# Optimization experiments

Hardware: AMD Instinct MI355X
Metric: run time of the kernel (lower is better)

Reference implementation:

```python
import jax, jax.numpy as jnp
import numpy as np


def conv1x1(x, w, b):
    # x: [B,C,H,W], w: [O,C], b: [O] -> [B,O,H,W]
    return jnp.einsum('bchw,oc->bohw', x, w) + b[None, :, None, None]


def maxpool2x2(x):
    B, C, H, W = x.shape
    return x.reshape(B, C, H // 2, 2, W // 2, 2).max(axis=(3, 5))


def setup_inputs() -> dict:
    key = jax.random.key(0)
    ks = jax.random.split(key, 10)
    C = 256
    x = jax.random.normal(ks[0], (16, C, 64, 64), dtype=jnp.float32)
    s = lambda fan_in: 1.0 / np.sqrt(fan_in)
    w_theta = jax.random.normal(ks[1], (C // 8, C), dtype=jnp.float32) * s(C)
    b_theta = jax.random.normal(ks[2], (C // 8,), dtype=jnp.float32) * 0.01
    w_phi = jax.random.normal(ks[3], (C // 8, C), dtype=jnp.float32) * s(C)
    b_phi = jax.random.normal(ks[4], (C // 8,), dtype=jnp.float32) * 0.01
    w_g = jax.random.normal(ks[5], (C // 2, C), dtype=jnp.float32) * s(C)
    b_g = jax.random.normal(ks[6], (C // 2,), dtype=jnp.float32) * 0.01
    w_attn = jax.random.normal(ks[7], (C, C // 2), dtype=jnp.float32) * s(C // 2)
    b_attn = jax.random.normal(ks[8], (C,), dtype=jnp.float32) * 0.01
    sigma = jnp.full((1,), 0.5, dtype=jnp.float32)
    return {"x": x, "w_theta": w_theta, "b_theta": b_theta,
            "w_phi": w_phi, "b_phi": b_phi, "w_g": w_g, "b_g": b_g,
            "w_attn": w_attn, "b_attn": b_attn, "sigma": sigma}


def reference(x, w_theta, b_theta, w_phi, b_phi, w_g, b_g, w_attn, b_attn, sigma):
    B, C, W, H = x.shape
    N = W * H
    N4 = N // 4
    # Q: [B, N, C/8]
    theta = conv1x1(x, w_theta, b_theta).reshape(B, C // 8, N).transpose(0, 2, 1)
    # K: [B, C/8, N/4] (2x2 maxpool downsample)
    phi = maxpool2x2(conv1x1(x, w_phi, b_phi)).reshape(B, C // 8, N4)
    # attention: [B, N, N/4]
    attn = jax.nn.softmax(jnp.einsum('bnc,bcm->bnm', theta, phi), axis=-1)
    # V: [B, N/4, C/2]
    g = maxpool2x2(conv1x1(x, w_g, b_g)).reshape(B, C // 2, N4).transpose(0, 2, 1)
    attn_g = jnp.einsum('bnm,bmc->bnc', attn, g).transpose(0, 2, 1).reshape(B, C // 2, W, H)
    attn_g = conv1x1(attn_g, w_attn, b_attn)
    return x + sigma[0] * attn_g
```

## Files before the change

kernel.cpp:

```cpp
#include <hip/hip_runtime.h>
#include <math.h>

#define BATCH 16
#define CIN   256
#define NPIX  4096
#define NP4   1024
#define DQK   32
#define DV    128
#define KT    64
#define QW    32
#define QT    128

typedef __attribute__((ext_vector_type(8)))  short short8v;
typedef __attribute__((ext_vector_type(16))) float f32x16;

#define ZERO16 {0.f,0.f,0.f,0.f,0.f,0.f,0.f,0.f,0.f,0.f,0.f,0.f,0.f,0.f,0.f,0.f}
#define LOG2E 1.44269504088896340736f
#define MFIX 64.0f

__device__ __forceinline__ unsigned short f2bf(float f) {
    unsigned u = __float_as_uint(f);
    u += 0x7FFFu + ((u >> 16) & 1u);
    return (unsigned short)(u >> 16);
}

__device__ __forceinline__ unsigned cvtpk(float a, float b) {
    unsigned r;
    asm("v_cvt_pk_bf16_f32 %0, %1, %2" : "=v"(r) : "v"(a), "v"(b));
    return r;
}

__device__ __forceinline__ short8v ldg8(const unsigned short* p) {
    return *(const short8v*)p;
}

#define PLSWAP(a, b) asm("v_permlane32_swap_b32 %0, %1" : "+v"(a), "+v"(b))

__global__ void wcvt_k(const float* __restrict__ wt, const float* __restrict__ wp,
                       const float* __restrict__ wg, const float* __restrict__ wa,
                       unsigned short* __restrict__ wqkv, unsigned short* __restrict__ wab)
{
    int i = blockIdx.x * 256 + threadIdx.x;
    if (i < 192 * 256) {
        int row = i >> 8, c = i & 255;
        float v = row < 32 ? wt[row * 256 + c]
                : row < 64 ? wp[(row - 32) * 256 + c]
                           : wg[(row - 64) * 256 + c];
        wqkv[i] = f2bf(v);
    } else {
        int j = i - 192 * 256;
        if (j < 256 * DV) wab[j] = f2bf(wa[j]);
    }
}

__global__ __launch_bounds__(256, 2) void conv_qkv_k(
    const float* __restrict__ x, const unsigned short* __restrict__ wqkv,
    const float* __restrict__ b_theta, const float* __restrict__ b_phi,
    const float* __restrict__ b_g, unsigned short* __restrict__ Qg,
    unsigned short* __restrict__ Kg, unsigned short* __restrict__ Vg)
{
    __shared__ __align__(16) union {
        unsigned short xs[2][2][128][8];
        float pool[2][160][32];
    } u;

    const int b    = blockIdx.y;
    const int tile = blockIdx.x;
    const int pixb = tile * 128;
    const int t    = threadIdx.x;
    const int wv   = t >> 6, l = t & 63, h = l >> 5, q31 = l & 31;
    const int sp   = t & 127, skb = t >> 7;

    const float* xb = x + (size_t)b * CIN * NPIX + pixb + sp;

    f32x16 acc[6];
#pragma unroll
    for (int i = 0; i < 6; ++i) acc[i] = ZERO16;

    float xa[8], xbr[8];
#pragma unroll
    for (int j = 0; j < 8; ++j) xa[j] = xb[(size_t)(skb * 8 + j) * NPIX];
    {
        unsigned pk[4];
#pragma unroll
        for (int jj = 0; jj < 4; ++jj) pk[jj] = cvtpk(xa[2*jj], xa[2*jj+1]);
        *(uint4*)&u.xs[0][skb][sp][0] = *(uint4*)pk;
    }
#pragma unroll
    for (int j = 0; j < 8; ++j) xbr[j] = xb[(size_t)(16 + skb * 8 + j) * NPIX];
    __syncthreads();

    for (int ks = 0; ks < 16; ks += 2) {
        if (ks < 14) {
            const float* xn = xb + (size_t)((ks + 2) * 16 + skb * 8) * NPIX;
#pragma unroll
            for (int j = 0; j < 8; ++j) xa[j] = xn[(size_t)j * NPIX];
        }
        {
            short8v bf = *(const short8v*)&u.xs[0][h][wv * 32 + q31][0];
#pragma unroll
            for (int rb = 0; rb < 6; ++rb) {
                short8v af = *(const short8v*)&wqkv[(size_t)(rb * 32 + q31) * 256 + ks * 16 + h * 8];
                acc[rb] = __builtin_amdgcn_mfma_f32_32x32x16_bf16(af, bf, acc[rb], 0, 0, 0);
            }
        }
        {
            unsigned pk[4];
#pragma unroll
            for (int jj = 0; jj < 4; ++jj) pk[jj] = cvtpk(xbr[2*jj], xbr[2*jj+1]);
            *(uint4*)&u.xs[1][skb][sp][0] = *(uint4*)pk;
        }
        __syncthreads();

        if (ks < 14) {
            const float* xn = xb + (size_t)((ks + 3) * 16 + skb * 8) * NPIX;
#pragma unroll
            for (int j = 0; j < 8; ++j) xbr[j] = xn[(size_t)j * NPIX];
        }
        {
            short8v bf = *(const short8v*)&u.xs[1][h][wv * 32 + q31][0];
#pragma unroll
            for (int rb = 0; rb < 6; ++rb) {
                short8v af = *(const short8v*)&wqkv[(size_t)(rb * 32 + q31) * 256 + (ks + 1) * 16 + h * 8];
                acc[rb] = __builtin_amdgcn_mfma_f32_32x32x16_bf16(af, bf, acc[rb], 0, 0, 0);
            }
        }
        if (ks < 14) {
            unsigned pk[4];
#pragma unroll
            for (int jj = 0; jj < 4; ++jj) pk[jj] = cvtpk(xa[2*jj], xa[2*jj+1]);
            *(uint4*)&u.xs[0][skb][sp][0] = *(uint4*)pk;
        }
        __syncthreads();
    }

    {
        int pix = pixb + wv * 32 + q31;
        unsigned short* qout = &Qg[((size_t)b * NPIX + pix) * DQK];
#pragma unroll
        for (int m = 0; m < 4; ++m) {
            unsigned pk2[2];
            float v0 = (acc[0][m*4+0] + b_theta[4*h + 8*m + 0]) * LOG2E;
            float v1 = (acc[0][m*4+1] + b_theta[4*h + 8*m + 1]) * LOG2E;
            float v2 = (acc[0][m*4+2] + b_theta[4*h + 8*m + 2]) * LOG2E;
            float v3 = (acc[0][m*4+3] + b_theta[4*h + 8*m + 3]) * LOG2E;
            pk2[0] = cvtpk(v0, v1);
            pk2[1] = cvtpk(v2, v3);
            *(uint2*)&qout[8*m + 4*h] = *(uint2*)pk2;
        }
    }

#pragma unroll
    for (int rb = 1; rb < 6; ++rb) {
#pragma unroll
        for (int r = 0; r < 16; ++r) {
            float v  = acc[rb][r];
            float o  = __shfl_xor(v, 1);
            float mx = fmaxf(v, o);
            if ((q31 & 1) == 0) {
                int row = (r & 3) + 8 * (r >> 2) + 4 * h;
                u.pool[wv >> 1][(rb - 1) * 32 + row][(wv & 1) * 16 + (q31 >> 1)] = mx;
            }
        }
    }
    __syncthreads();

    {
        int wx = t & 31;
        int pp = tile * 32 + wx;
#pragma unroll
        for (int i = 0; i < 20; ++i) {
            int ch = (t >> 5) * 20 + i;
            float v = fmaxf(u.pool[0][ch][wx], u.pool[1][ch][wx]);
            if (ch < 32) {
                v += b_phi[ch];
                Kg[(((size_t)b * 4 + (ch >> 3)) * NP4 + pp) * 8 + (ch & 7)] = f2bf(v);
            } else {
                int c = ch - 32;
                v += b_g[c];
                Vg[((size_t)b * 128 + (pp >> 3)) * (DV * 8) + (size_t)c * 8 + (pp & 7)] = f2bf(v);
            }
        }
    }
}

__global__ __launch_bounds__(256, 2) void flash_k(
    const unsigned short* __restrict__ Qg, const unsigned short* __restrict__ Kg,
    const unsigned short* __restrict__ Vg, const unsigned short* __restrict__ wab,
    const float* __restrict__ b_attn, const float* __restrict__ sigma,
    const float* __restrict__ x, float* __restrict__ out)
{
    __shared__ __align__(16) unsigned short os[4][16 * QW * 8];

    const int b   = blockIdx.y;
    const int t   = threadIdx.x;
    const int wv  = t >> 6;
    const int l   = t & 63;
    const int h   = l >> 5;
    const int q31 = l & 31;
    const int p0  = blockIdx.x * QT + wv * QW;

    const unsigned short* Kp = Kg + (size_t)b * 4 * NP4 * 8 + ((size_t)h * NP4 + q31) * 8;
    const unsigned short* Vp = Vg + (size_t)b * 128 * DV * 8 + h * 1024 + q31 * 8;

    short8v qf0 = ldg8(&Qg[((size_t)b * NPIX + p0 + q31) * DQK + h * 8]);
    short8v qf1 = ldg8(&Qg[((size_t)b * NPIX + p0 + q31) * DQK + 16 + h * 8]);

    f32x16 o0 = ZERO16, o1 = ZERO16, o2 = ZERO16, o3 = ZERO16;
    float lsum = 0.f;

    short8v kfA[4], kfB[4], vg[16];
#pragma unroll
    for (int i = 0; i < 4; ++i)
        kfA[i] = ldg8(Kp + (i >> 1) * (2 * NP4 * 8) + (i & 1) * 256);
#pragma unroll
    for (int g = 0; g < 4; ++g)
#pragma unroll
        for (int cc = 0; cc < 4; ++cc)
            vg[g * 4 + cc] = ldg8(Vp + g * 2048 + cc * 256);

    auto tile = [&](int kt, short8v (&kfc)[4], short8v (&kfn)[4], bool pref) {
        f32x16 s0 = ZERO16, s1 = ZERO16;
        __builtin_amdgcn_s_setprio(1);
        s0 = __builtin_amdgcn_mfma_f32_32x32x16_bf16(kfc[0], qf0, s0, 0, 0, 0);
        s1 = __builtin_amdgcn_mfma_f32_32x32x16_bf16(kfc[1], qf0, s1, 0, 0, 0);
        s0 = __builtin_amdgcn_mfma_f32_32x32x16_bf16(kfc[2], qf1, s0, 0, 0, 0);
        s1 = __builtin_amdgcn_mfma_f32_32x32x16_bf16(kfc[3], qf1, s1, 0, 0, 0);
        __builtin_amdgcn_s_setprio(0);

        if (pref) {
            const unsigned short* kp1 = Kp + (size_t)(kt + 1) * 512;
#pragma unroll
            for (int i = 0; i < 4; ++i)
                kfn[i] = ldg8(kp1 + (i >> 1) * (2 * NP4 * 8) + (i & 1) * 256);
        }

        float ts[16];
#pragma unroll
        for (int r = 0; r < 16; ++r) {
            s0[r] = exp2f(s0[r] - MFIX);
            s1[r] = exp2f(s1[r] - MFIX);
            ts[r] = s0[r] + s1[r];
        }
#pragma unroll
        for (int d = 8; d >= 1; d >>= 1)
#pragma unroll
            for (int r = 0; r < d; ++r) ts[r] += ts[r + d];
        lsum += ts[0] + __shfl_xor(ts[0], 32);

        unsigned ca[8], cb[8];
#pragma unroll
        for (int j = 0; j < 8; ++j) {
            ca[j] = cvtpk(s0[2*j], s0[2*j+1]);
            cb[j] = cvtpk(s1[2*j], s1[2*j+1]);
        }
        PLSWAP(ca[0], ca[2]); PLSWAP(ca[1], ca[3]);
        PLSWAP(ca[4], ca[6]); PLSWAP(ca[5], ca[7]);
        PLSWAP(cb[0], cb[2]); PLSWAP(cb[1], cb[3]);
        PLSWAP(cb[4], cb[6]); PLSWAP(cb[5], cb[7]);
        union { unsigned uu[4]; short8v v; } pa[4];
#pragma unroll
        for (int j = 0; j < 4; ++j) {
            pa[0].uu[j] = ca[j];     pa[1].uu[j] = ca[4 + j];
            pa[2].uu[j] = cb[j];     pa[3].uu[j] = cb[4 + j];
        }

        const unsigned short* vp1 = Vp + (size_t)(kt + 1) * 8192;
#pragma unroll
        for (int g = 0; g < 4; ++g) {
            __builtin_amdgcn_s_setprio(1);
            o0 = __builtin_amdgcn_mfma_f32_32x32x16_bf16(pa[g].v, vg[g*4+0], o0, 0, 0, 0);
            o1 = __builtin_amdgcn_mfma_f32_32x32x16_bf16(pa[g].v, vg[g*4+1], o1, 0, 0, 0);
            o2 = __builtin_amdgcn_mfma_f32_32x32x16_bf16(pa[g].v, vg[g*4+2], o2, 0, 0, 0);
            o3 = __builtin_amdgcn_mfma_f32_32x32x16_bf16(pa[g].v, vg[g*4+3], o3, 0, 0, 0);
            __builtin_amdgcn_s_setprio(0);
            if (pref) {
#pragma unroll
                for (int cc = 0; cc < 4; ++cc)
                    vg[g*4+cc] = ldg8(vp1 + g * 2048 + cc * 256);
            }
        }
    };

    for (int kt = 0; kt < 16; kt += 2) {
        tile(kt,     kfA, kfB, true);
        tile(kt + 1, kfB, kfA, kt + 1 < 15);
    }

    float rinv = 1.0f / lsum;
    unsigned short* osw = os[wv];
#pragma unroll
    for (int r = 0; r < 16; ++r) {
        int q = (r & 3) + 8 * (r >> 2) + 4 * h;
        float rn = __shfl(rinv, q);
        osw[((0 * 4 + (q31 >> 3)) * QW + q) * 8 + (l & 7)] = f2bf(o0[r] * rn);
        osw[((1 * 4 + (q31 >> 3)) * QW + q) * 8 + (l & 7)] = f2bf(o1[r] * rn);
        osw[((2 * 4 + (q31 >> 3)) * QW + q) * 8 + (l & 7)] = f2bf(o2[r] * rn);
        osw[((3 * 4 + (q31 >> 3)) * QW + q) * 8 + (l & 7)] = f2bf(o3[r] * rn);
    }

    const float sg = sigma[0];
    for (int cht = 0; cht < 8; ++cht) {
        f32x16 e = ZERO16;
#pragma unroll
        for (int ks16 = 0; ks16 < 8; ++ks16) {
            short8v wf = ldg8(&wab[(size_t)(cht * 32 + q31) * DV + ks16 * 16 + h * 8]);
            short8v of = *(const short8v*)&osw[((ks16 * 2 + h) * QW + q31) * 8];
            e = __builtin_amdgcn_mfma_f32_32x32x16_bf16(wf, of, e, 0, 0, 0);
        }
#pragma unroll
        for (int r = 0; r < 16; ++r) {
            int ch = cht * 32 + (r & 3) + 8 * (r >> 2) + 4 * h;
            size_t idx = ((size_t)b * 256 + ch) * NPIX + p0 + q31;
            out[idx] = fmaf(sg, e[r] + b_attn[ch], x[idx]);
        }
    }
}

extern "C" void kernel_launch(void* const* d_in, const int* in_sizes, int n_in,
                              void* d_out, int out_size, void* d_ws, size_t ws_size,
                              hipStream_t stream) {
    const float* x       = (const float*)d_in[0];
    const float* w_theta = (const float*)d_in[1];
    const float* b_theta = (const float*)d_in[2];
    const float* w_phi   = (const float*)d_in[3];
    const float* b_phi   = (const float*)d_in[4];
    const float* w_g     = (const float*)d_in[5];
    const float* b_g     = (const float*)d_in[6];
    const float* w_attn  = (const float*)d_in[7];
    const float* b_attn  = (const float*)d_in[8];
    const float* sigma   = (const float*)d_in[9];
    float* out = (float*)d_out;

    unsigned short* Qg   = (unsigned short*)d_ws;
    unsigned short* Kg   = Qg + (size_t)BATCH * NPIX * DQK;
    unsigned short* Vg   = Kg + (size_t)BATCH * 4 * NP4 * 8;
    unsigned short* wab  = Vg + (size_t)BATCH * 128 * DV * 8;
    unsigned short* wqkv = wab + (size_t)256 * DV;

    wcvt_k    <<<dim3((192 * 256 + 256 * DV + 255) / 256), 256, 0, stream>>>(
        w_theta, w_phi, w_g, w_attn, wqkv, wab);
    conv_qkv_k<<<dim3(NPIX / 128, BATCH), 256, 0, stream>>>(
        x, wqkv, b_theta, b_phi, b_g, Qg, Kg, Vg);
    flash_k   <<<dim3(NPIX / QT, BATCH), 256, 0, stream>>>(
        Qg, Kg, Vg, wab, b_attn, sigma, x, out);
}
```

Before: 102.9 us.

## Split output projection out of flash kernel into separate coalesced conv kernel

```diff
diff --git a/kernel.cpp b/kernel.cpp
--- a/kernel.cpp
+++ b/kernel.cpp
@@ -186,11 +186,9 @@
 
 __global__ __launch_bounds__(256, 2) void flash_k(
     const unsigned short* __restrict__ Qg, const unsigned short* __restrict__ Kg,
-    const unsigned short* __restrict__ Vg, const unsigned short* __restrict__ wab,
-    const float* __restrict__ b_attn, const float* __restrict__ sigma,
-    const float* __restrict__ x, float* __restrict__ out)
+    const unsigned short* __restrict__ Vg, unsigned short* __restrict__ Og)
 {
-    __shared__ __align__(16) unsigned short os[4][16 * QW * 8];
+    __shared__ __align__(16) unsigned short os[4][16 * 33 * 8];
 
     const int b   = blockIdx.y;
     const int t   = threadIdx.x;
@@ -221,12 +219,10 @@
 
     auto tile = [&](int kt, short8v (&kfc)[4], short8v (&kfn)[4], bool pref) {
         f32x16 s0 = ZERO16, s1 = ZERO16;
-        __builtin_amdgcn_s_setprio(1);
         s0 = __builtin_amdgcn_mfma_f32_32x32x16_bf16(kfc[0], qf0, s0, 0, 0, 0);
         s1 = __builtin_amdgcn_mfma_f32_32x32x16_bf16(kfc[1], qf0, s1, 0, 0, 0);
         s0 = __builtin_amdgcn_mfma_f32_32x32x16_bf16(kfc[2], qf1, s0, 0, 0, 0);
         s1 = __builtin_amdgcn_mfma_f32_32x32x16_bf16(kfc[3], qf1, s1, 0, 0, 0);
-        __builtin_amdgcn_s_setprio(0);
 
         if (pref) {
             const unsigned short* kp1 = Kp + (size_t)(kt + 1) * 512;
@@ -268,12 +264,10 @@
         const unsigned short* vp1 = Vp + (size_t)(kt + 1) * 8192;
 #pragma unroll
         for (int g = 0; g < 4; ++g) {
-            __builtin_amdgcn_s_setprio(1);
             o0 = __builtin_amdgcn_mfma_f32_32x32x16_bf16(pa[g].v, vg[g*4+0], o0, 0, 0, 0);
             o1 = __builtin_amdgcn_mfma_f32_32x32x16_bf16(pa[g].v, vg[g*4+1], o1, 0, 0, 0);
             o2 = __builtin_amdgcn_mfma_f32_32x32x16_bf16(pa[g].v, vg[g*4+2], o2, 0, 0, 0);
             o3 = __builtin_amdgcn_mfma_f32_32x32x16_bf16(pa[g].v, vg[g*4+3], o3, 0, 0, 0);
-            __builtin_amdgcn_s_setprio(0);
             if (pref) {
 #pragma unroll
                 for (int cc = 0; cc < 4; ++cc)
@@ -293,27 +287,84 @@
     for (int r = 0; r < 16; ++r) {
         int q = (r & 3) + 8 * (r >> 2) + 4 * h;
         float rn = __shfl(rinv, q);
-        osw[((0 * 4 + (q31 >> 3)) * QW + q) * 8 + (l & 7)] = f2bf(o0[r] * rn);
-        osw[((1 * 4 + (q31 >> 3)) * QW + q) * 8 + (l & 7)] = f2bf(o1[r] * rn);
-        osw[((2 * 4 + (q31 >> 3)) * QW + q) * 8 + (l & 7)] = f2bf(o2[r] * rn);
-        osw[((3 * 4 + (q31 >> 3)) * QW + q) * 8 + (l & 7)] = f2bf(o3[r] * rn);
-    }
+        int e = l & 7;
+        osw[(((q31 >> 3)     ) * 33 + q) * 8 + e] = f2bf(o0[r] * rn);
+        osw[(((q31 >> 3) +  4) * 33 + q) * 8 + e] = f2bf(o1[r] * rn);
+        osw[(((q31 >> 3) +  8) * 33 + q) * 8 + e] = f2bf(o2[r] * rn);
+        osw[(((q31 >> 3) + 12) * 33 + q) * 8 + e] = f2bf(o3[r] * rn);
+    }
+    {
+        unsigned short* og = Og + ((size_t)b * NPIX + p0) * DV;
+        int cb = l & 15, qof = l >> 4;
+#pragma unroll
+        for (int j = 0; j < 8; ++j) {
+            int q = j * 4 + qof;
+            short8v v = *(const short8v*)&osw[(cb * 33 + q) * 8];
+            *(short8v*)&og[(size_t)q * DV + cb * 8] = v;
+        }
+    }
+}
+
+__global__ __launch_bounds__(256, 2) void conv_out_k(
+    const unsigned short* __restrict__ Og, const unsigned short* __restrict__ wab,
+    const float* __restrict__ b_attn, const float* __restrict__ sigma,
+    const float* __restrict__ x, float* __restrict__ out)
+{
+    __shared__ __align__(16) float ls[32][132];
+
+    const int b   = blockIdx.z;
+    const int chH = blockIdx.y;
+    const int px0 = blockIdx.x * 128;
+    const int t   = threadIdx.x;
+    const int wv  = t >> 6;
+    const int l   = t & 63;
+    const int h   = l >> 5;
+    const int q31 = l & 31;
+    const int pxw = px0 + wv * 32;
+
+    const unsigned short* ob = Og + ((size_t)b * NPIX + pxw + q31) * DV;
+    short8v of[8];
+#pragma unroll
+    for (int k = 0; k < 8; ++k) of[k] = ldg8(ob + k * 16 + h * 8);
+
+    f32x16 e[4];
+#pragma unroll
+    for (int i = 0; i < 4; ++i) e[i] = ZERO16;
+    const unsigned short* wb = wab + (size_t)(chH * 128) * DV;
+#pragma unroll
+    for (int chb = 0; chb < 4; ++chb)
+#pragma unroll
+        for (int k = 0; k < 8; ++k) {
+            short8v wf = ldg8(wb + (size_t)(chb * 32 + q31) * DV + k * 16 + h * 8);
+            e[chb] = __builtin_amdgcn_mfma_f32_32x32x16_bf16(wf, of[k], e[chb], 0, 0, 0);
+        }
 
     const float sg = sigma[0];
-    for (int cht = 0; cht < 8; ++cht) {
-        f32x16 e = ZERO16;
-#pragma unroll
-        for (int ks16 = 0; ks16 < 8; ++ks16) {
-            short8v wf = ldg8(&wab[(size_t)(cht * 32 + q31) * DV + ks16 * 16 + h * 8]);
-            short8v of = *(const short8v*)&osw[((ks16 * 2 + h) * QW + q31) * 8];
-            e = __builtin_amdgcn_mfma_f32_32x32x16_bf16(wf, of, e, 0, 0, 0);
-        }
+#pragma unroll 1
+    for (int chb = 0; chb < 4; ++chb) {
 #pragma unroll
         for (int r = 0; r < 16; ++r) {
-            int ch = cht * 32 + (r & 3) + 8 * (r >> 2) + 4 * h;
-            size_t idx = ((size_t)b * 256 + ch) * NPIX + p0 + q31;
-            out[idx] = fmaf(sg, e[r] + b_attn[ch], x[idx]);
-        }
+            int crow = (r & 3) + 8 * (r >> 2) + 4 * h;
+            ls[crow][wv * 32 + q31] = e[chb][r];
+        }
+        __syncthreads();
+#pragma unroll
+        for (int rep = 0; rep < 4; ++rep) {
+            int cl  = rep * 8 + (t >> 5);
+            int ch  = chH * 128 + chb * 32 + cl;
+            int px4 = (t & 31) * 4;
+            float4 v = *(const float4*)&ls[cl][px4];
+            float bias = b_attn[ch];
+            size_t idx = ((size_t)b * 256 + ch) * NPIX + px0 + px4;
+            float4 xv = *(const float4*)&x[idx];
+            float4 o;
+            o.x = fmaf(sg, v.x + bias, xv.x);
+            o.y = fmaf(sg, v.y + bias, xv.y);
+            o.z = fmaf(sg, v.z + bias, xv.z);
+            o.w = fmaf(sg, v.w + bias, xv.w);
+            *(float4*)&out[idx] = o;
+        }
+        __syncthreads();
     }
 }
 
@@ -337,11 +388,13 @@
     unsigned short* Vg   = Kg + (size_t)BATCH * 4 * NP4 * 8;
     unsigned short* wab  = Vg + (size_t)BATCH * 128 * DV * 8;
     unsigned short* wqkv = wab + (size_t)256 * DV;
+    unsigned short* Og   = wqkv + (size_t)192 * 256;
 
     wcvt_k    <<<dim3((192 * 256 + 256 * DV + 255) / 256), 256, 0, stream>>>(
         w_theta, w_phi, w_g, w_attn, wqkv, wab);
     conv_qkv_k<<<dim3(NPIX / 128, BATCH), 256, 0, stream>>>(
         x, wqkv, b_theta, b_phi, b_g, Qg, Kg, Vg);
-    flash_k   <<<dim3(NPIX / QT, BATCH), 256, 0, stream>>>(
-        Qg, Kg, Vg, wab, b_attn, sigma, x, out);
-}
+    flash_k   <<<dim3(NPIX / QT, BATCH), 256, 0, stream>>>(Qg, Kg, Vg, Og);
+    conv_out_k<<<dim3(NPIX / 128, 2, BATCH), 256, 0, stream>>>(
+        Og, wab, b_attn, sigma, x, out);
+}
```

Result: slower. 142.4 us (+38.5%).

## Stage epilogue through LDS for float4 output stores and pad O tile

Applied to the files above, without the earlier changes.

```diff
diff --git a/kernel.cpp b/kernel.cpp
--- a/kernel.cpp
+++ b/kernel.cpp
@@ -7,7 +7,6 @@
 #define NP4   1024
 #define DQK   32
 #define DV    128
-#define KT    64
 #define QW    32
 #define QT    128
 
@@ -190,15 +189,17 @@
     const float* __restrict__ b_attn, const float* __restrict__ sigma,
     const float* __restrict__ x, float* __restrict__ out)
 {
-    __shared__ __align__(16) unsigned short os[4][16 * QW * 8];
-
-    const int b   = blockIdx.y;
-    const int t   = threadIdx.x;
-    const int wv  = t >> 6;
-    const int l   = t & 63;
-    const int h   = l >> 5;
-    const int q31 = l & 31;
-    const int p0  = blockIdx.x * QT + wv * QW;
+    __shared__ __align__(16) unsigned short os[4][16 * 33 * 8];
+    __shared__ __align__(16) float ls[32][132];
+
+    const int b    = blockIdx.y;
+    const int t    = threadIdx.x;
+    const int wv   = t >> 6;
+    const int l    = t & 63;
+    const int h    = l >> 5;
+    const int q31  = l & 31;
+    const int pxblk = blockIdx.x * QT;
+    const int p0   = pxblk + wv * QW;
 
     const unsigned short* Kp = Kg + (size_t)b * 4 * NP4 * 8 + ((size_t)h * NP4 + q31) * 8;
     const unsigned short* Vp = Vg + (size_t)b * 128 * DV * 8 + h * 1024 + q31 * 8;
@@ -221,12 +222,10 @@
 
     auto tile = [&](int kt, short8v (&kfc)[4], short8v (&kfn)[4], bool pref) {
         f32x16 s0 = ZERO16, s1 = ZERO16;
-        __builtin_amdgcn_s_setprio(1);
         s0 = __builtin_amdgcn_mfma_f32_32x32x16_bf16(kfc[0], qf0, s0, 0, 0, 0);
         s1 = __builtin_amdgcn_mfma_f32_32x32x16_bf16(kfc[1], qf0, s1, 0, 0, 0);
         s0 = __builtin_amdgcn_mfma_f32_32x32x16_bf16(kfc[2], qf1, s0, 0, 0, 0);
         s1 = __builtin_amdgcn_mfma_f32_32x32x16_bf16(kfc[3], qf1, s1, 0, 0, 0);
-        __builtin_amdgcn_s_setprio(0);
 
         if (pref) {
             const unsigned short* kp1 = Kp + (size_t)(kt + 1) * 512;
@@ -268,12 +267,10 @@
         const unsigned short* vp1 = Vp + (size_t)(kt + 1) * 8192;
 #pragma unroll
         for (int g = 0; g < 4; ++g) {
-            __builtin_amdgcn_s_setprio(1);
             o0 = __builtin_amdgcn_mfma_f32_32x32x16_bf16(pa[g].v, vg[g*4+0], o0, 0, 0, 0);
             o1 = __builtin_amdgcn_mfma_f32_32x32x16_bf16(pa[g].v, vg[g*4+1], o1, 0, 0, 0);
             o2 = __builtin_amdgcn_mfma_f32_32x32x16_bf16(pa[g].v, vg[g*4+2], o2, 0, 0, 0);
             o3 = __builtin_amdgcn_mfma_f32_32x32x16_bf16(pa[g].v, vg[g*4+3], o3, 0, 0, 0);
-            __builtin_amdgcn_s_setprio(0);
             if (pref) {
 #pragma unroll
                 for (int cc = 0; cc < 4; ++cc)
@@ -293,27 +290,53 @@
     for (int r = 0; r < 16; ++r) {
         int q = (r & 3) + 8 * (r >> 2) + 4 * h;
         float rn = __shfl(rinv, q);
-        osw[((0 * 4 + (q31 >> 3)) * QW + q) * 8 + (l & 7)] = f2bf(o0[r] * rn);
-        osw[((1 * 4 + (q31 >> 3)) * QW + q) * 8 + (l & 7)] = f2bf(o1[r] * rn);
-        osw[((2 * 4 + (q31 >> 3)) * QW + q) * 8 + (l & 7)] = f2bf(o2[r] * rn);
-        osw[((3 * 4 + (q31 >> 3)) * QW + q) * 8 + (l & 7)] = f2bf(o3[r] * rn);
+        int e8 = l & 7;
+        osw[(((q31 >> 3)     ) * 33 + q) * 8 + e8] = f2bf(o0[r] * rn);
+        osw[(((q31 >> 3) +  4) * 33 + q) * 8 + e8] = f2bf(o1[r] * rn);
+        osw[(((q31 >> 3) +  8) * 33 + q) * 8 + e8] = f2bf(o2[r] * rn);
+        osw[(((q31 >> 3) + 12) * 33 + q) * 8 + e8] = f2bf(o3[r] * rn);
     }
 
     const float sg = sigma[0];
+    const int cl8  = t >> 5;
+    const int px4  = (t & 31) * 4;
+#pragma unroll 1
     for (int cht = 0; cht < 8; ++cht) {
+        float4 xv[4];
+#pragma unroll
+        for (int rep = 0; rep < 4; ++rep) {
+            int ch = cht * 32 + rep * 8 + cl8;
+            xv[rep] = *(const float4*)&x[((size_t)b * 256 + ch) * NPIX + pxblk + px4];
+        }
+
         f32x16 e = ZERO16;
 #pragma unroll
         for (int ks16 = 0; ks16 < 8; ++ks16) {
             short8v wf = ldg8(&wab[(size_t)(cht * 32 + q31) * DV + ks16 * 16 + h * 8]);
-            short8v of = *(const short8v*)&osw[((ks16 * 2 + h) * QW + q31) * 8];
+            short8v of = *(const short8v*)&osw[((ks16 * 2 + h) * 33 + q31) * 8];
             e = __builtin_amdgcn_mfma_f32_32x32x16_bf16(wf, of, e, 0, 0, 0);
         }
 #pragma unroll
         for (int r = 0; r < 16; ++r) {
-            int ch = cht * 32 + (r & 3) + 8 * (r >> 2) + 4 * h;
-            size_t idx = ((size_t)b * 256 + ch) * NPIX + p0 + q31;
-            out[idx] = fmaf(sg, e[r] + b_attn[ch], x[idx]);
-        }
+            int crow = (r & 3) + 8 * (r >> 2) + 4 * h;
+            ls[crow][wv * 32 + q31] = e[r];
+        }
+        __syncthreads();
+#pragma unroll
+        for (int rep = 0; rep < 4; ++rep) {
+            int cl = rep * 8 + cl8;
+            int ch = cht * 32 + cl;
+            float4 v = *(const float4*)&ls[cl][px4];
+            float bias = b_attn[ch];
+            size_t idx = ((size_t)b * 256 + ch) * NPIX + pxblk + px4;
+            float4 o;
+            o.x = fmaf(sg, v.x + bias, xv[rep].x);
+            o.y = fmaf(sg, v.y + bias, xv[rep].y);
+            o.z = fmaf(sg, v.z + bias, xv[rep].z);
+            o.w = fmaf(sg, v.w + bias, xv[rep].w);
+            *(float4*)&out[idx] = o;
+        }
+        __syncthreads();
     }
 }
 
```

Result: no change. 104.4 us (+1.4%).
